# Performance work log

Hardware: AMD Instinct MI355X
Metric: run time of the kernel (lower is better)

Reference implementation:

```python
import jax, jax.numpy as jnp
import numpy as np

B, TQ, TK = 4, 128, 512
DQ = DK = DV = H = 1024


def setup_inputs() -> dict:
    key = jax.random.key(0)
    ks = jax.random.split(key, 7)
    s = 0.05  # keep tanh out of saturation
    return {
        "query": jax.random.normal(ks[0], (B, TQ, DQ), dtype=jnp.float32),
        "key": jax.random.normal(ks[1], (B, TK, DK), dtype=jnp.float32),
        "value": jax.random.normal(ks[2], (B, TK, DV), dtype=jnp.float32),
        "Wq": jax.random.normal(ks[3], (DQ, H), dtype=jnp.float32) * s,
        "bq": jax.random.normal(ks[4], (H,), dtype=jnp.float32) * s,
        "Wk": jax.random.normal(ks[5], (DK, H), dtype=jnp.float32) * s,
        "v": jax.random.normal(ks[6], (H,), dtype=jnp.float32) * s,
    }


def reference(query, key, value, Wq, bq, Wk, v):
    # additive (Bahdanau) attention
    wq = jnp.einsum("bqd,dh->bqh", query, Wq) + bq      # [B,Tq,H]
    uh = jnp.einsum("bkd,dh->bkh", key, Wk)             # [B,Tk,H]
    # broadcast add -> [B,Tq,Tk,H], tanh, project to scalar score
    scores = jnp.einsum("bqkh,h->bqk",
                        jnp.tanh(wq[:, :, None, :] + uh[:, None, :, :]), v)
    attn = jax.nn.softmax(scores, axis=-1)              # [B,Tq,Tk]
    h = jnp.einsum("bqk,bkv->bqv", attn, value)         # [B,Tq,Dv]
    return h, attn
```

## Files before the change

### kernel.cpp

```cpp
#include <hip/hip_runtime.h>
#include <hip/hip_bf16.h>

typedef float f32x4 __attribute__((ext_vector_type(4)));
typedef float f32x2 __attribute__((ext_vector_type(2)));
typedef short s16x8 __attribute__((ext_vector_type(8)));
typedef short s16x4 __attribute__((ext_vector_type(4)));

#define NB  4
#define NTQ 128
#define NTK 512
#define NH  1024
#define ECLAMP 3.0e4f

__device__ __forceinline__ unsigned short f2bf(float x) {
    unsigned u = __builtin_bit_cast(unsigned, x);
    u += 0x7FFFu + ((u >> 16) & 1u);
    return (unsigned short)(u >> 16);
}

#define K2E  2.8853900817779268f

#define GLD16(gp, lp) __builtin_amdgcn_global_load_lds( \
    (const __attribute__((address_space(1))) unsigned int*)(gp), \
    (__attribute__((address_space(3))) unsigned int*)(lp), 16, 0, 0)

__global__ __launch_bounds__(256) void prep_kernel(
    const float* __restrict__ Q, const float* __restrict__ K,
    const float* __restrict__ Wq, const float* __restrict__ Wk,
    const float* __restrict__ value,
    short* __restrict__ Qb, short* __restrict__ Kb,
    short* __restrict__ WqT, short* __restrict__ WkT, short* __restrict__ valT)
{
    const int t = threadIdx.x, bx = blockIdx.x;
    if (bx < 640) {
        const float* src; short* dst; size_t base;
        if (bx < 128) { src = Q; dst = Qb; base = (size_t)bx * 4096; }
        else          { src = K; dst = Kb; base = (size_t)(bx - 128) * 4096; }
        #pragma unroll
        for (int i = 0; i < 4; ++i) {
            const size_t off = base + (size_t)(i * 256 + t) * 4;
            const float4 vv = *(const float4*)(src + off);
            s16x4 o = { (short)f2bf(vv.x), (short)f2bf(vv.y),
                        (short)f2bf(vv.z), (short)f2bf(vv.w) };
            *(s16x4*)(dst + off) = o;
        }
        return;
    }
    __shared__ float tile[64][65];
    const int i = bx - 640;
    const float* src; short* dst; int Cs, Rs, r0, c0;
    if (i < 256)      { src = Wq; dst = WqT; Cs = 1024; Rs = 1024; r0 = (i >> 4) * 64; c0 = (i & 15) * 64; }
    else if (i < 512) { const int j = i - 256; src = Wk; dst = WkT; Cs = 1024; Rs = 1024; r0 = (j >> 4) * 64; c0 = (j & 15) * 64; }
    else {
        const int j = i - 512, b = j >> 7, ti = j & 127;
        src = value + (size_t)b * 512 * 1024; dst = valT + (size_t)b * 1024 * 512;
        Cs = 1024; Rs = 512; r0 = (ti >> 4) * 64; c0 = (ti & 15) * 64;
    }
    {
        const int c = (t & 15) * 4;
        #pragma unroll
        for (int it = 0; it < 4; ++it) {
            const int r = (t >> 4) + it * 16;
            const float4 vv = *(const float4*)(src + (size_t)(r0 + r) * Cs + c0 + c);
            tile[r][c + 0] = vv.x; tile[r][c + 1] = vv.y;
            tile[r][c + 2] = vv.z; tile[r][c + 3] = vv.w;
        }
    }
    __syncthreads();
    {
        const int r = (t & 15) * 4;
        #pragma unroll
        for (int it = 0; it < 4; ++it) {
            const int c = (t >> 4) + it * 16;
            s16x4 o = { (short)f2bf(tile[r + 0][c]), (short)f2bf(tile[r + 1][c]),
                        (short)f2bf(tile[r + 2][c]), (short)f2bf(tile[r + 3][c]) };
            *(s16x4*)(dst + (size_t)(c0 + c) * Rs + r0 + r) = o;
        }
    }
}

__global__ __launch_bounds__(256) void mm_kernel(
    const short* __restrict__ Qb, const short* __restrict__ Kb,
    const short* __restrict__ WqT, const short* __restrict__ WkT,
    const float* __restrict__ bq,
    float* __restrict__ Ea_out, unsigned short* __restrict__ EbT)
{
    __shared__ short ldsA[2][128][64];
    __shared__ short ldsB[2][64][64];
    const int t = threadIdx.x;
    const int bx0 = blockIdx.x;
    const int bx = (bx0 & 7) * 40 + (bx0 >> 3);
    const bool g1 = bx < 64;
    const short *A, *B; int m0, n0;
    if (g1) { A = Qb; B = WqT; m0 = (bx >> 4) * 128; n0 = (bx & 15) * 64; }
    else    { const int i = bx - 64; A = Kb; B = WkT; m0 = (i >> 4) * 128; n0 = (i & 15) * 64; }
    A += (size_t)m0 * 1024; B += (size_t)n0 * 1024;

    f32x4 acc[4][2];
    #pragma unroll
    for (int i = 0; i < 4; ++i)
        #pragma unroll
        for (int j = 0; j < 2; ++j) acc[i][j] = f32x4{0.f, 0.f, 0.f, 0.f};

    const int lane = t & 63, wid = t >> 6;
    const int wr = wid >> 1, wc = wid & 1;
    const int fr = lane & 15, fko = (lane >> 4) * 16;

    #define STAGE_MM(buf, k0) do {                                              \
        _Pragma("unroll")                                                       \
        for (int it = 0; it < 4; ++it) {                                        \
            const int idx = it * 256 + t;                                       \
            const int row = idx >> 3, c16 = idx & 7;                            \
            const int sc = c16 ^ (row & 7);                                     \
            GLD16(A + (size_t)row * 1024 + (k0) + sc * 8,                       \
                  &ldsA[buf][0][0] + idx * 8);                                  \
        }                                                                       \
        _Pragma("unroll")                                                       \
        for (int it = 0; it < 2; ++it) {                                        \
            const int idx = it * 256 + t;                                       \
            const int row = idx >> 3, c16 = idx & 7;                            \
            const int sc = c16 ^ (row & 7);                                     \
            GLD16(B + (size_t)row * 1024 + (k0) + sc * 8,                       \
                  &ldsB[buf][0][0] + idx * 8);                                  \
        }                                                                       \
    } while (0)

    #define COMPUTE_MM(buf) do {                                                \
        _Pragma("unroll")                                                       \
        for (int kk = 0; kk < 2; ++kk) {                                        \
            s16x8 af[4], bfv[2];                                                \
            _Pragma("unroll")                                                   \
            for (int i = 0; i < 4; ++i) {                                       \
                const int rowA = wr * 64 + i * 16 + fr;                         \
                int offA = rowA * 128 + kk * 64 + fko; offA ^= (rowA & 7) << 4; \
                af[i] = *(const s16x8*)((const char*)&ldsA[buf][0][0] + offA);  \
            }                                                                   \
            _Pragma("unroll")                                                   \
            for (int ni = 0; ni < 2; ++ni) {                                    \
                const int rowB = wc * 32 + ni * 16 + fr;                        \
                int offB = rowB * 128 + kk * 64 + fko; offB ^= (rowB & 7) << 4; \
                bfv[ni] = *(const s16x8*)((const char*)&ldsB[buf][0][0] + offB);\
            }                                                                   \
            _Pragma("unroll")                                                   \
            for (int mi = 0; mi < 4; ++mi)                                      \
                _Pragma("unroll")                                               \
                for (int ni = 0; ni < 2; ++ni)                                  \
                    acc[mi][ni] = __builtin_amdgcn_mfma_f32_16x16x32_bf16(      \
                                      af[mi], bfv[ni], acc[mi][ni], 0, 0, 0);   \
        }                                                                       \
    } while (0)

    STAGE_MM(0, 0);
    __syncthreads();
    int cur = 0;
    for (int s = 0; s < 15; ++s) {
        STAGE_MM(cur ^ 1, (s + 1) * 64);
        COMPUTE_MM(cur);
        __syncthreads();
        cur ^= 1;
    }
    COMPUTE_MM(cur);

    const int row0 = (lane >> 4) * 4;
    if (g1) {
        #pragma unroll
        for (int ni = 0; ni < 2; ++ni) {
            const int n = n0 + wc * 32 + ni * 16 + fr;
            const float bias = bq[n];
            #pragma unroll
            for (int mi = 0; mi < 4; ++mi) {
                const int m = m0 + wr * 64 + mi * 16 + row0;
                #pragma unroll
                for (int j = 0; j < 4; ++j)
                    Ea_out[(size_t)(m + j) * 1024 + n] =
                        fminf(__builtin_amdgcn_exp2f(K2E * (acc[mi][ni][j] + bias)), ECLAMP);
            }
        }
    } else {
        #pragma unroll
        for (int mi = 0; mi < 4; ++mi) {
            const int m = m0 + wr * 64 + mi * 16 + row0;
            const int b = m >> 9, kk = m & 511;
            #pragma unroll
            for (int ni = 0; ni < 2; ++ni) {
                const int n = n0 + wc * 32 + ni * 16 + fr;
                s16x4 ev;
                #pragma unroll
                for (int j = 0; j < 4; ++j)
                    ev[j] = (short)f2bf(fminf(__builtin_amdgcn_exp2f(K2E * acc[mi][ni][j]), ECLAMP));
                *(s16x4*)&EbT[((size_t)b * 1024 + n) * 512 + kk] = ev;
            }
        }
    }
    #undef STAGE_MM
    #undef COMPUTE_MM
}

__global__ __launch_bounds__(1024, 8) void scores_softmax(
    const unsigned short* __restrict__ EbT, const float* __restrict__ Ea,
    const float* __restrict__ v,
    float* __restrict__ attn_out, short* __restrict__ attnb)
{
    __shared__ float2 s_eav[1024];
    __shared__ float  s_part[8][512];
    __shared__ float  s_red[16];
    const int t = threadIdx.x, bx = blockIdx.x;
    const int b = bx & 3;
    const int q = bx >> 2;
    const int bq = b * 128 + q;
    const int kq = t & 127;
    const int hs = t >> 7;
    const int lane = t & 63, wid = t >> 6;

    s_eav[t] = make_float2(Ea[(size_t)bq * 1024 + t], v[t]);
    __syncthreads();

    const int h0 = hs * 128;
    const uint2* up = (const uint2*)(EbT + ((size_t)(b * 1024 + h0)) * 512) + kq;
    f32x2 alo = {0.f, 0.f}, ahi = {0.f, 0.f};
    const f32x2 one2 = {1.f, 1.f};

    #pragma unroll 2
    for (int hg = 0; hg < 32; ++hg) {
        const int hb = hg * 4;
        const uint2 r0 = up[(size_t)(hb + 0) * 128];
        const uint2 r1 = up[(size_t)(hb + 1) * 128];
        const uint2 r2 = up[(size_t)(hb + 2) * 128];
        const uint2 r3 = up[(size_t)(hb + 3) * 128];
        const float2 ev0 = s_eav[h0 + hb + 0];
        const float2 ev1 = s_eav[h0 + hb + 1];
        const float2 ev2 = s_eav[h0 + hb + 2];
        const float2 ev3 = s_eav[h0 + hb + 3];
        #define UNPK(r) f32x2{__builtin_bit_cast(float, (r) << 16),            \
                              __builtin_bit_cast(float, (r) & 0xFFFF0000u)}
        const f32x2 b0lo = UNPK(r0.x), b0hi = UNPK(r0.y);
        const f32x2 b1lo = UNPK(r1.x), b1hi = UNPK(r1.y);
        const f32x2 b2lo = UNPK(r2.x), b2hi = UNPK(r2.y);
        const f32x2 b3lo = UNPK(r3.x), b3hi = UNPK(r3.y);
        #undef UNPK
        const f32x2 e0 = {ev0.x, ev0.x}, e1 = {ev1.x, ev1.x};
        const f32x2 e2 = {ev2.x, ev2.x}, e3 = {ev3.x, ev3.x};
        const f32x2 vv0 = {ev0.y, ev0.y}, vv1 = {ev1.y, ev1.y};
        const f32x2 vv2 = {ev2.y, ev2.y}, vv3 = {ev3.y, ev3.y};

        #define GRPPK(accv, B0, B1, B2, B3) do {                                \
            const f32x2 u0 = B0 * e0 + one2;                                    \
            const f32x2 u1 = B1 * e1 + one2;                                    \
            const f32x2 u2 = B2 * e2 + one2;                                    \
            const f32x2 u3 = B3 * e3 + one2;                                    \
            const f32x2 d01 = u0 * u1, d23 = u2 * u3;                           \
            f32x2 n01 = vv0 * u1; n01 = vv1 * u0 + n01;                         \
            f32x2 n23 = vv2 * u3; n23 = vv3 * u2 + n23;                         \
            f32x2 n = n01 * d23; n = n23 * d01 + n;                             \
            const f32x2 den = d01 * d23;                                        \
            const f32x2 r = {__builtin_amdgcn_rcpf(den.x),                      \
                             __builtin_amdgcn_rcpf(den.y)};                     \
            accv = n * r + accv;                                                \
        } while (0)

        GRPPK(alo, b0lo, b1lo, b2lo, b3lo);
        GRPPK(ahi, b0hi, b1hi, b2hi, b3hi);
        #undef GRPPK
    }
    *(f32x4*)&s_part[hs][kq * 4] = f32x4{alo.x, alo.y, ahi.x, ahi.y};
    __syncthreads();

    const int kk = t & 511;
    float z = 0.f;
    #pragma unroll
    for (int j = 0; j < 8; ++j) z += s_part[j][kk];
    z *= -2.0f;

    float m = z;
    #pragma unroll
    for (int off = 32; off > 0; off >>= 1)
        m = fmaxf(m, __shfl_xor(m, off, 64));
    if (lane == 0) s_red[wid] = m;
    __syncthreads();
    float mx = s_red[0];
    #pragma unroll
    for (int w = 1; w < 8; ++w) mx = fmaxf(mx, s_red[w]);
    const float p = __expf(z - mx);
    __syncthreads();

    float sl = p;
    #pragma unroll
    for (int off = 32; off > 0; off >>= 1)
        sl += __shfl_xor(sl, off, 64);
    if (lane == 0) s_red[wid] = sl;
    __syncthreads();
    float s = 0.f;
    #pragma unroll
    for (int w = 0; w < 8; ++w) s += s_red[w];

    if (t < 512) {
        const float a = p * (1.0f / s);
        attn_out[(size_t)bq * 512 + kk] = a;
        attnb[(size_t)bq * 512 + kk] = (short)f2bf(a);
    }
}

__global__ __launch_bounds__(256) void pv_gemm(
    const short* __restrict__ attnb, const short* __restrict__ valT,
    float* __restrict__ outh)
{
    __shared__ short ldsA[2][128][64];
    __shared__ short ldsB[2][64][64];
    const int t = threadIdx.x, bx = blockIdx.x;
    const int b = bx >> 4, nt = bx & 15;
    const int n0 = nt * 64;
    const short* A = attnb + (size_t)b * 128 * 512;
    const short* B = valT + (size_t)b * 1024 * 512 + (size_t)n0 * 512;

    f32x4 acc[4][2];
    #pragma unroll
    for (int i = 0; i < 4; ++i)
        #pragma unroll
        for (int j = 0; j < 2; ++j) acc[i][j] = f32x4{0.f, 0.f, 0.f, 0.f};

    const int lane = t & 63, wid = t >> 6;
    const int wr = wid >> 1, wc = wid & 1;
    const int fr = lane & 15, fko = (lane >> 4) * 16;

    #define STAGE_PV(buf, k0) do {                                              \
        _Pragma("unroll")                                                       \
        for (int it = 0; it < 4; ++it) {                                        \
            const int idx = it * 256 + t;                                       \
            const int row = idx >> 3, c16 = idx & 7;                            \
            const int sc = c16 ^ (row & 7);                                     \
            GLD16(A + (size_t)row * 512 + (k0) + sc * 8,                        \
                  &ldsA[buf][0][0] + idx * 8);                                  \
        }                                                                       \
        _Pragma("unroll")                                                       \
        for (int it = 0; it < 2; ++it) {                                        \
            const int idx = it * 256 + t;                                       \
            const int row = idx >> 3, c16 = idx & 7;                            \
            const int sc = c16 ^ (row & 7);                                     \
            GLD16(B + (size_t)row * 512 + (k0) + sc * 8,                        \
                  &ldsB[buf][0][0] + idx * 8);                                  \
        }                                                                       \
    } while (0)

    #define COMPUTE_PV(buf) do {                                                \
        _Pragma("unroll")                                                       \
        for (int kk = 0; kk < 2; ++kk) {                                        \
            s16x8 af[4], bfv[2];                                                \
            _Pragma("unroll")                                                   \
            for (int i = 0; i < 4; ++i) {                                       \
                const int rowA = wr * 64 + i * 16 + fr;                         \
                int offA = rowA * 128 + kk * 64 + fko; offA ^= (rowA & 7) << 4; \
                af[i] = *(const s16x8*)((const char*)&ldsA[buf][0][0] + offA);  \
            }                                                                   \
            _Pragma("unroll")                                                   \
            for (int ni = 0; ni < 2; ++ni) {                                    \
                const int rowB = wc * 32 + ni * 16 + fr;                        \
                int offB = rowB * 128 + kk * 64 + fko; offB ^= (rowB & 7) << 4; \
                bfv[ni] = *(const s16x8*)((const char*)&ldsB[buf][0][0] + offB);\
            }                                                                   \
            _Pragma("unroll")                                                   \
            for (int mi = 0; mi < 4; ++mi)                                      \
                _Pragma("unroll")                                               \
                for (int ni = 0; ni < 2; ++ni)                                  \
                    acc[mi][ni] = __builtin_amdgcn_mfma_f32_16x16x32_bf16(      \
                                      af[mi], bfv[ni], acc[mi][ni], 0, 0, 0);   \
        }                                                                       \
    } while (0)

    STAGE_PV(0, 0);
    __syncthreads();
    int cur = 0;
    for (int s = 0; s < 7; ++s) {
        STAGE_PV(cur ^ 1, (s + 1) * 64);
        COMPUTE_PV(cur);
        __syncthreads();
        cur ^= 1;
    }
    COMPUTE_PV(cur);

    const int row0 = (lane >> 4) * 4;
    #pragma unroll
    for (int ni = 0; ni < 2; ++ni) {
        const int n = n0 + wc * 32 + ni * 16 + fr;
        #pragma unroll
        for (int mi = 0; mi < 4; ++mi) {
            const int m = wr * 64 + mi * 16 + row0;
            #pragma unroll
            for (int j = 0; j < 4; ++j)
                outh[(size_t)(b * 128 + m + j) * 1024 + n] = acc[mi][ni][j];
        }
    }
    #undef STAGE_PV
    #undef COMPUTE_PV
}

extern "C" void kernel_launch(void* const* d_in, const int* in_sizes, int n_in,
                              void* d_out, int out_size, void* d_ws, size_t ws_size,
                              hipStream_t stream)
{
    const float* query = (const float*)d_in[0];
    const float* key   = (const float*)d_in[1];
    const float* value = (const float*)d_in[2];
    const float* Wq    = (const float*)d_in[3];
    const float* bq    = (const float*)d_in[4];
    const float* Wk    = (const float*)d_in[5];
    const float* v     = (const float*)d_in[6];
    float* out = (float*)d_out;

    char* w = (char*)d_ws;
    float*          ws_Ea  = (float*)w;
    unsigned short* ws_EbT = (unsigned short*)(w + (2u << 20));
    short* Qb     = (short*)(w + (6u << 20));
    short* Kb     = (short*)(w + (7u << 20));
    short* WqT    = (short*)(w + (11u << 20));
    short* WkT    = (short*)(w + (13u << 20));
    short* valT   = (short*)(w + (15u << 20));
    short* attnb  = (short*)(w + (19u << 20));

    float* out_h    = out;
    float* out_attn = out + (size_t)NB * NTQ * NH;

    prep_kernel   <<<dim3(1664), dim3(256),  0, stream>>>(query, key, Wq, Wk, value,
                                                          Qb, Kb, WqT, WkT, valT);
    mm_kernel     <<<dim3(320),  dim3(256),  0, stream>>>(Qb, Kb, WqT, WkT, bq, ws_Ea, ws_EbT);
    scores_softmax<<<dim3(512),  dim3(1024), 0, stream>>>(ws_EbT, ws_Ea, v, out_attn, attnb);
    pv_gemm       <<<dim3(64),   dim3(256),  0, stream>>>(attnb, valT, out_h);
}
```

Baseline: 72.57 us.

## Tile score kernel over 8 queries per block and split softmax into own kernel

The score kernel now handles 8 query rows and a 128-key slice per block, so each loaded bf16 EbT element is reused across 8 queries instead of one. This cuts the repeated global reads of the 4MB EbT tensor by about 8x. Because a block no longer sees a full key row, the softmax moves into a separate kernel that reads z from a workspace buffer. That adds a launch and a small round trip of z through global memory.

```diff
diff --git a/kernel.cpp b/kernel.cpp
--- a/kernel.cpp
+++ b/kernel.cpp
@@ -196,58 +196,66 @@
     #undef COMPUTE_MM
 }
 
-__global__ __launch_bounds__(1024, 8) void scores_softmax(
+__global__ __launch_bounds__(512, 4) void scores_z(
     const unsigned short* __restrict__ EbT, const float* __restrict__ Ea,
-    const float* __restrict__ v,
-    float* __restrict__ attn_out, short* __restrict__ attnb)
-{
-    __shared__ float2 s_eav[1024];
-    __shared__ float  s_part[8][512];
-    __shared__ float  s_red[16];
+    const float* __restrict__ v, float* __restrict__ zout)
+{
+    __shared__ float4 s_eaA[1024];
+    __shared__ float4 s_eaB[1024];
+    __shared__ float  s_v[1024];
+    __shared__ float  s_part[8][8][128];
     const int t = threadIdx.x, bx = blockIdx.x;
-    const int b = bx & 3;
-    const int q = bx >> 2;
-    const int bq = b * 128 + q;
-    const int kq = t & 127;
-    const int hs = t >> 7;
-    const int lane = t & 63, wid = t >> 6;
-
-    s_eav[t] = make_float2(Ea[(size_t)bq * 1024 + t], v[t]);
+    const int b = bx & 3, kq4 = (bx >> 2) & 3, q8 = bx >> 4;
+    const int bq0 = b * 128 + q8 * 8;
+    const int kp = t & 63;
+    const int hs = t >> 6;
+
+    for (int h = t; h < 1024; h += 512) {
+        s_eaA[h] = make_float4(Ea[(size_t)(bq0 + 0) * 1024 + h],
+                               Ea[(size_t)(bq0 + 1) * 1024 + h],
+                               Ea[(size_t)(bq0 + 2) * 1024 + h],
+                               Ea[(size_t)(bq0 + 3) * 1024 + h]);
+        s_eaB[h] = make_float4(Ea[(size_t)(bq0 + 4) * 1024 + h],
+                               Ea[(size_t)(bq0 + 5) * 1024 + h],
+                               Ea[(size_t)(bq0 + 6) * 1024 + h],
+                               Ea[(size_t)(bq0 + 7) * 1024 + h]);
+        s_v[h] = v[h];
+    }
     __syncthreads();
 
     const int h0 = hs * 128;
-    const uint2* up = (const uint2*)(EbT + ((size_t)(b * 1024 + h0)) * 512) + kq;
-    f32x2 alo = {0.f, 0.f}, ahi = {0.f, 0.f};
+    const unsigned* up = (const unsigned*)(EbT + ((size_t)(b * 1024 + h0)) * 512)
+                         + kq4 * 64 + kp;
+    f32x2 a0 = {0.f,0.f}, a1 = {0.f,0.f}, a2 = {0.f,0.f}, a3 = {0.f,0.f};
+    f32x2 a4 = {0.f,0.f}, a5 = {0.f,0.f}, a6 = {0.f,0.f}, a7 = {0.f,0.f};
     const f32x2 one2 = {1.f, 1.f};
 
     #pragma unroll 2
     for (int hg = 0; hg < 32; ++hg) {
         const int hb = hg * 4;
-        const uint2 r0 = up[(size_t)(hb + 0) * 128];
-        const uint2 r1 = up[(size_t)(hb + 1) * 128];
-        const uint2 r2 = up[(size_t)(hb + 2) * 128];
-        const uint2 r3 = up[(size_t)(hb + 3) * 128];
-        const float2 ev0 = s_eav[h0 + hb + 0];
-        const float2 ev1 = s_eav[h0 + hb + 1];
-        const float2 ev2 = s_eav[h0 + hb + 2];
-        const float2 ev3 = s_eav[h0 + hb + 3];
+        const unsigned r0 = up[(size_t)(hb + 0) * 256];
+        const unsigned r1 = up[(size_t)(hb + 1) * 256];
+        const unsigned r2 = up[(size_t)(hb + 2) * 256];
+        const unsigned r3 = up[(size_t)(hb + 3) * 256];
         #define UNPK(r) f32x2{__builtin_bit_cast(float, (r) << 16),            \
                               __builtin_bit_cast(float, (r) & 0xFFFF0000u)}
-        const f32x2 b0lo = UNPK(r0.x), b0hi = UNPK(r0.y);
-        const f32x2 b1lo = UNPK(r1.x), b1hi = UNPK(r1.y);
-        const f32x2 b2lo = UNPK(r2.x), b2hi = UNPK(r2.y);
-        const f32x2 b3lo = UNPK(r3.x), b3hi = UNPK(r3.y);
+        const f32x2 eb0 = UNPK(r0), eb1 = UNPK(r1);
+        const f32x2 eb2 = UNPK(r2), eb3 = UNPK(r3);
         #undef UNPK
-        const f32x2 e0 = {ev0.x, ev0.x}, e1 = {ev1.x, ev1.x};
-        const f32x2 e2 = {ev2.x, ev2.x}, e3 = {ev3.x, ev3.x};
-        const f32x2 vv0 = {ev0.y, ev0.y}, vv1 = {ev1.y, ev1.y};
-        const f32x2 vv2 = {ev2.y, ev2.y}, vv3 = {ev3.y, ev3.y};
-
-        #define GRPPK(accv, B0, B1, B2, B3) do {                                \
-            const f32x2 u0 = B0 * e0 + one2;                                    \
-            const f32x2 u1 = B1 * e1 + one2;                                    \
-            const f32x2 u2 = B2 * e2 + one2;                                    \
-            const f32x2 u3 = B3 * e3 + one2;                                    \
+        const float4 eA0 = s_eaA[h0 + hb + 0], eA1 = s_eaA[h0 + hb + 1];
+        const float4 eA2 = s_eaA[h0 + hb + 2], eA3 = s_eaA[h0 + hb + 3];
+        const float4 eB0 = s_eaB[h0 + hb + 0], eB1 = s_eaB[h0 + hb + 1];
+        const float4 eB2 = s_eaB[h0 + hb + 2], eB3 = s_eaB[h0 + hb + 3];
+        const float vw0 = s_v[h0 + hb + 0], vw1 = s_v[h0 + hb + 1];
+        const float vw2 = s_v[h0 + hb + 2], vw3 = s_v[h0 + hb + 3];
+        const f32x2 vv0 = {vw0, vw0}, vv1 = {vw1, vw1};
+        const f32x2 vv2 = {vw2, vw2}, vv3 = {vw3, vw3};
+
+        #define GRPPK(accv, E0, E1, E2, E3) do {                                \
+            const f32x2 u0 = eb0 * f32x2{E0, E0} + one2;                        \
+            const f32x2 u1 = eb1 * f32x2{E1, E1} + one2;                        \
+            const f32x2 u2 = eb2 * f32x2{E2, E2} + one2;                        \
+            const f32x2 u3 = eb3 * f32x2{E3, E3} + one2;                        \
             const f32x2 d01 = u0 * u1, d23 = u2 * u3;                           \
             f32x2 n01 = vv0 * u1; n01 = vv1 * u0 + n01;                         \
             f32x2 n23 = vv2 * u3; n23 = vv3 * u2 + n23;                         \
@@ -258,18 +266,45 @@
             accv = n * r + accv;                                                \
         } while (0)
 
-        GRPPK(alo, b0lo, b1lo, b2lo, b3lo);
-        GRPPK(ahi, b0hi, b1hi, b2hi, b3hi);
+        GRPPK(a0, eA0.x, eA1.x, eA2.x, eA3.x);
+        GRPPK(a1, eA0.y, eA1.y, eA2.y, eA3.y);
+        GRPPK(a2, eA0.z, eA1.z, eA2.z, eA3.z);
+        GRPPK(a3, eA0.w, eA1.w, eA2.w, eA3.w);
+        GRPPK(a4, eB0.x, eB1.x, eB2.x, eB3.x);
+        GRPPK(a5, eB0.y, eB1.y, eB2.y, eB3.y);
+        GRPPK(a6, eB0.z, eB1.z, eB2.z, eB3.z);
+        GRPPK(a7, eB0.w, eB1.w, eB2.w, eB3.w);
         #undef GRPPK
     }
-    *(f32x4*)&s_part[hs][kq * 4] = f32x4{alo.x, alo.y, ahi.x, ahi.y};
-    __syncthreads();
-
-    const int kk = t & 511;
-    float z = 0.f;
-    #pragma unroll
-    for (int j = 0; j < 8; ++j) z += s_part[j][kk];
-    z *= -2.0f;
+    *(f32x2*)&s_part[hs][0][kp * 2] = a0;
+    *(f32x2*)&s_part[hs][1][kp * 2] = a1;
+    *(f32x2*)&s_part[hs][2][kp * 2] = a2;
+    *(f32x2*)&s_part[hs][3][kp * 2] = a3;
+    *(f32x2*)&s_part[hs][4][kp * 2] = a4;
+    *(f32x2*)&s_part[hs][5][kp * 2] = a5;
+    *(f32x2*)&s_part[hs][6][kp * 2] = a6;
+    *(f32x2*)&s_part[hs][7][kp * 2] = a7;
+    __syncthreads();
+
+    #pragma unroll
+    for (int rep = 0; rep < 2; ++rep) {
+        const int idx = rep * 512 + t;
+        const int qq = idx >> 7, kk = idx & 127;
+        float z = 0.f;
+        #pragma unroll
+        for (int j = 0; j < 8; ++j) z += s_part[j][qq][kk];
+        zout[(size_t)(bq0 + qq) * 512 + kq4 * 128 + kk] = -2.0f * z;
+    }
+}
+
+__global__ __launch_bounds__(512) void softmax_kernel(
+    const float* __restrict__ zin, float* __restrict__ attn_out,
+    short* __restrict__ attnb)
+{
+    __shared__ float s_red[16];
+    const int t = threadIdx.x, bqi = blockIdx.x;
+    const float z = zin[(size_t)bqi * 512 + t];
+    const int lane = t & 63, wid = t >> 6;
 
     float m = z;
     #pragma unroll
@@ -293,11 +328,9 @@
     #pragma unroll
     for (int w = 0; w < 8; ++w) s += s_red[w];
 
-    if (t < 512) {
-        const float a = p * (1.0f / s);
-        attn_out[(size_t)bq * 512 + kk] = a;
-        attnb[(size_t)bq * 512 + kk] = (short)f2bf(a);
-    }
+    const float a = p * (1.0f / s);
+    attn_out[(size_t)bqi * 512 + t] = a;
+    attnb[(size_t)bqi * 512 + t] = (short)f2bf(a);
 }
 
 __global__ __launch_bounds__(256) void pv_gemm(
@@ -415,13 +448,15 @@
     short* WkT    = (short*)(w + (13u << 20));
     short* valT   = (short*)(w + (15u << 20));
     short* attnb  = (short*)(w + (19u << 20));
+    float* zbuf   = (float*)(w + (20u << 20));
 
     float* out_h    = out;
     float* out_attn = out + (size_t)NB * NTQ * NH;
 
-    prep_kernel   <<<dim3(1664), dim3(256),  0, stream>>>(query, key, Wq, Wk, value,
-                                                          Qb, Kb, WqT, WkT, valT);
-    mm_kernel     <<<dim3(320),  dim3(256),  0, stream>>>(Qb, Kb, WqT, WkT, bq, ws_Ea, ws_EbT);
-    scores_softmax<<<dim3(512),  dim3(1024), 0, stream>>>(ws_EbT, ws_Ea, v, out_attn, attnb);
-    pv_gemm       <<<dim3(64),   dim3(256),  0, stream>>>(attnb, valT, out_h);
-}
+    prep_kernel   <<<dim3(1664), dim3(256), 0, stream>>>(query, key, Wq, Wk, value,
+                                                         Qb, Kb, WqT, WkT, valT);
+    mm_kernel     <<<dim3(320),  dim3(256), 0, stream>>>(Qb, Kb, WqT, WkT, bq, ws_Ea, ws_EbT);
+    scores_z      <<<dim3(256),  dim3(512), 0, stream>>>(ws_EbT, ws_Ea, v, zbuf);
+    softmax_kernel<<<dim3(512),  dim3(512), 0, stream>>>(zbuf, out_attn, attnb);
+    pv_gemm       <<<dim3(64),   dim3(256), 0, stream>>>(attnb, valT, out_h);
+}
```

After: 67.94 us, median of 2. -6.4%, faster.
